# Optimization experiments

Measured on AMD Instinct MI355X. Metric: run time of the kernel, lower is better.

The kernel has to match this reference:

```python
import jax, jax.numpy as jnp
import numpy as np

D_MODEL = 1024
N_EXPERTS = 8
TOP_K = 2
LN_EPS = 1e-5


def setup_inputs() -> dict:
    key = jax.random.key(0)
    ks = jax.random.split(key, 8)
    B, S, d, E = 2, 2048, D_MODEL, N_EXPERTS
    f = 2 * d
    s_in = 0.02
    return {
        "x": jax.random.normal(ks[0], (B, S, d), jnp.float32),
        "Wg": jax.random.normal(ks[1], (d, E), jnp.float32) * s_in,
        "bg": jnp.zeros((E,), jnp.float32),
        "W1": jax.random.normal(ks[2], (E, d, f), jnp.float32) * s_in,
        "b1": jnp.zeros((E, f), jnp.float32),
        "W2": jax.random.normal(ks[3], (E, f, d), jnp.float32) * s_in,
        "b2": jnp.zeros((E, d), jnp.float32),
        "gamma": jnp.ones((d,), jnp.float32),
        "beta": jnp.zeros((d,), jnp.float32),
    }


def reference(x, Wg, bg, W1, b1, W2, b2, gamma, beta):
    # Gating + top-k routing (softmax over the selected top-k logits only)
    logits = jnp.einsum("bsd,de->bse", x, Wg) + bg            # [B,S,E]
    topk_vals, topk_idx = jax.lax.top_k(logits, TOP_K)         # [B,S,K]
    topk_w = jax.nn.softmax(topk_vals, axis=-1)                # [B,S,K]

    # Expert MLPs evaluated densely for all experts (dropout is identity in eval)
    h = jax.nn.relu(jnp.einsum("bsd,edf->bsef", x, W1) + b1)   # [B,S,E,2d]
    eo = jnp.einsum("bsef,efd->bsed", h, W2) + b2              # [B,S,E,d]

    # Gather the top-k experts' outputs per token and combine with gate weights
    sel = jnp.take_along_axis(eo, topk_idx[..., None], axis=2)  # [B,S,K,d]
    mixed = jnp.sum(sel * topk_w[..., None], axis=2)            # [B,S,d]

    # Residual + LayerNorm
    y = mixed + x
    mu = jnp.mean(y, axis=-1, keepdims=True)
    var = jnp.mean(jnp.square(y - mu), axis=-1, keepdims=True)
    return gamma * (y - mu) * jax.lax.rsqrt(var + LN_EPS) + beta
```

## Files before the change

### kernel.cpp

```cpp
#include <hip/hip_runtime.h>


typedef unsigned short ushort_t;
typedef short short8 __attribute__((ext_vector_type(8)));
typedef float f32x4 __attribute__((ext_vector_type(4)));

#define T_TOKENS 4096
#define DMODEL 1024
#define FFN 2048
#define NEXP 8
#define MAXSLOTS 9216
#define GATE_BLOCKS 256
#define TOK_PER_BLK 16

__device__ __forceinline__ ushort_t f2bf(float f) {
    unsigned u = __float_as_uint(f);
    return (ushort_t)((u + 0x7fffu + ((u >> 16) & 1u)) >> 16);
}
__device__ __forceinline__ float bflo(unsigned packed) {
    return __uint_as_float(packed << 16);
}
__device__ __forceinline__ float bfhi(unsigned packed) {
    return __uint_as_float(packed & 0xffff0000u);
}

__device__ __forceinline__ void gload_lds16(const void* g, void* l) {
    __builtin_amdgcn_global_load_lds(
        (const __attribute__((address_space(1))) unsigned int*)g,
        (__attribute__((address_space(3))) unsigned int*)l,
        16, 0, 0);
}

__global__ void init_kernel(int* slot_token) {
    int i = blockIdx.x * 256 + threadIdx.x;
    if (i < MAXSLOTS) slot_token[i] = -1;
}

__global__ __launch_bounds__(256) void gate_kernel(
    const float* __restrict__ x, const float* __restrict__ Wg,
    const float* __restrict__ bg,
    int* __restrict__ top_idx, float* __restrict__ top_w,
    int* __restrict__ blk_hist)
{
    __shared__ int hist[NEXP];
    const int tid = threadIdx.x, lane = tid & 63, w = tid >> 6;
    if (tid < NEXP) hist[tid] = 0;
    __syncthreads();

    float wreg[16][8];
    #pragma unroll
    for (int i = 0; i < 16; i++) {
        const float4* wp = (const float4*)&Wg[(i * 64 + lane) * 8];
        float4 a = wp[0], b = wp[1];
        wreg[i][0] = a.x; wreg[i][1] = a.y; wreg[i][2] = a.z; wreg[i][3] = a.w;
        wreg[i][4] = b.x; wreg[i][5] = b.y; wreg[i][6] = b.z; wreg[i][7] = b.w;
    }
    float bgv[8];
    #pragma unroll
    for (int e = 0; e < 8; e++) bgv[e] = bg[e];

    const int t0 = blockIdx.x * TOK_PER_BLK + w * 4;
    #pragma unroll 1
    for (int it = 0; it < 4; it++) {
        int t = t0 + it;
        const float* xr = x + (size_t)t * DMODEL;
        float acc[8] = {0.f,0.f,0.f,0.f,0.f,0.f,0.f,0.f};
        #pragma unroll
        for (int i = 0; i < 16; i++) {
            float xv = xr[i * 64 + lane];
            #pragma unroll
            for (int e = 0; e < 8; e++) acc[e] += xv * wreg[i][e];
        }
        #pragma unroll
        for (int off = 32; off > 0; off >>= 1) {
            #pragma unroll
            for (int e = 0; e < 8; e++) acc[e] += __shfl_down(acc[e], off);
        }
        if (lane == 0) {
            float l[8];
            #pragma unroll
            for (int e = 0; e < 8; e++) l[e] = acc[e] + bgv[e];
            int i0 = 0; float v0 = l[0];
            #pragma unroll
            for (int e = 1; e < 8; e++) if (l[e] > v0) { v0 = l[e]; i0 = e; }
            int i1 = -1; float v1 = -1e30f;
            #pragma unroll
            for (int e = 0; e < 8; e++) if (e != i0 && l[e] > v1) { v1 = l[e]; i1 = e; }
            float eg = expf(v1 - v0);
            float den = 1.f + eg;
            int p0 = atomicAdd(&hist[i0], 1);
            int p1 = atomicAdd(&hist[i1], 1);
            top_idx[2 * t]     = i0 | (p0 << 4);
            top_idx[2 * t + 1] = i1 | (p1 << 4);
            top_w[2 * t]     = 1.f / den;
            top_w[2 * t + 1] = eg / den;
        }
    }
    __syncthreads();
    if (tid < NEXP) blk_hist[blockIdx.x * NEXP + tid] = hist[tid];
}

__global__ __launch_bounds__(512) void scan_kernel(
    const int* __restrict__ blk_hist, int* __restrict__ blk_base,
    int* __restrict__ offs)
{
    __shared__ int cnt[NEXP];
    const int tid = threadIdx.x, lane = tid & 63, e = tid >> 6;
    int carry = 0;
    #pragma unroll
    for (int r = 0; r < GATE_BLOCKS / 64; r++) {
        int b = r * 64 + lane;
        int orig = blk_hist[b * NEXP + e];
        int v = orig;
        #pragma unroll
        for (int off = 1; off < 64; off <<= 1) {
            int u = __shfl_up(v, off);
            if (lane >= off) v += u;
        }
        blk_base[b * NEXP + e] = carry + v - orig;
        carry += __shfl(v, 63);
    }
    if (lane == 0) cnt[e] = carry;
    __syncthreads();
    if (tid == 0) {
        int cum = 0;
        for (int ee = 0; ee < NEXP; ee++) {
            offs[ee] = cum;
            cum += (cnt[ee] + 127) & ~127;
        }
        offs[NEXP] = cum;
    }
}

__global__ void scatter_kernel(const int* __restrict__ top_idx,
                               const int* __restrict__ offs,
                               const int* __restrict__ blk_base,
                               int* __restrict__ slot_token,
                               int* __restrict__ slot_of)
{
    int t = blockIdx.x * 256 + threadIdx.x;
    if (t >= T_TOKENS) return;
    int gb = t / TOK_PER_BLK;
    #pragma unroll
    for (int k = 0; k < 2; k++) {
        int v = top_idx[2 * t + k];
        int e = v & 15;
        int pos = v >> 4;
        int slot = offs[e] + blk_base[gb * NEXP + e] + pos;
        slot_token[slot] = t;
        slot_of[2 * t + k] = slot;
    }
}

__global__ __launch_bounds__(256) void gather_kernel(
    const float* __restrict__ x, const int* __restrict__ slot_token,
    ushort_t* __restrict__ Xg)
{
    int row = blockIdx.x * 2 + (threadIdx.x >> 7);
    int c = threadIdx.x & 127;
    int tok = slot_token[row];
    uint4* dst = (uint4*)(Xg + (size_t)row * DMODEL) + c;
    if (tok < 0) {
        *dst = make_uint4(0, 0, 0, 0);
        return;
    }
    const float4* sx = (const float4*)(x + (size_t)tok * DMODEL) + c * 2;
    float4 a = sx[0], b = sx[1];
    uint4 o;
    o.x = f2bf(a.x) | ((unsigned)f2bf(a.y) << 16);
    o.y = f2bf(a.z) | ((unsigned)f2bf(a.w) << 16);
    o.z = f2bf(b.x) | ((unsigned)f2bf(b.y) << 16);
    o.w = f2bf(b.z) | ((unsigned)f2bf(b.w) << 16);
    *dst = o;
}

__global__ __launch_bounds__(256) void transpose_kernel(
    const float* __restrict__ src, ushort_t* __restrict__ dst, int R, int C)
{
    __shared__ ushort_t tile[64][68];
    const float* s = src + (size_t)blockIdx.z * R * C;
    ushort_t* d = dst + (size_t)blockIdx.z * R * C;
    int c0 = blockIdx.x * 64, r0 = blockIdx.y * 64;
    int fc = threadIdx.x & 15, rp = threadIdx.x >> 4;
    #pragma unroll
    for (int p = 0; p < 4; p++) {
        int r = p * 16 + rp;
        float4 v = *(const float4*)&s[(size_t)(r0 + r) * C + c0 + fc * 4];
        uint2 pk;
        pk.x = f2bf(v.x) | ((unsigned)f2bf(v.y) << 16);
        pk.y = f2bf(v.z) | ((unsigned)f2bf(v.w) << 16);
        *(uint2*)&tile[r][fc * 4] = pk;
    }
    __syncthreads();
    #pragma unroll
    for (int p = 0; p < 4; p++) {
        int c = p * 16 + rp;
        int rb = fc * 4;
        uint2 pk;
        pk.x = tile[rb + 0][c] | ((unsigned)tile[rb + 1][c] << 16);
        pk.y = tile[rb + 2][c] | ((unsigned)tile[rb + 3][c] << 16);
        *(uint2*)&d[(size_t)(c0 + c) * R + r0 + rb] = pk;
    }
}

template <int K, int N, bool RELU, typename OutT>
__global__ __launch_bounds__(256) void expert_gemm(
    const ushort_t* __restrict__ A,
    const ushort_t* __restrict__ Bt,
    const float* __restrict__ bias,
    OutT* __restrict__ Cout,
    const int* __restrict__ offs)
{
    const int e  = blockIdx.z;
    const int mt = blockIdx.y;
    const int nt = blockIdx.x;
    const int off_e = offs[e];
    const int Mpad  = offs[e + 1] - off_e;
    if (mt * 128 >= Mpad) return;

    __shared__ __align__(16) ushort_t As[128 * 32];
    __shared__ __align__(16) ushort_t Bs[128 * 32];

    const int tid  = threadIdx.x;
    const int lane = tid & 63;
    const int w    = tid >> 6;
    const int quad = lane >> 4;
    const int r16  = lane & 15;
    const int lrow = lane >> 2;
    const int lk   = (lane & 3) * 8;

    const size_t arow0 = (size_t)(off_e + mt * 128);
    const ushort_t* aS0 = A + (arow0 + (size_t)(2 * w + 0) * 16 + lrow) * K + lk;
    const ushort_t* aS1 = A + (arow0 + (size_t)(2 * w + 1) * 16 + lrow) * K + lk;
    const ushort_t* Bte = Bt + (size_t)e * N * K;
    const ushort_t* bS0 = Bte + ((size_t)(nt * 128 + (2 * w + 0) * 16 + lrow)) * K + lk;
    const ushort_t* bS1 = Bte + ((size_t)(nt * 128 + (2 * w + 1) * 16 + lrow)) * K + lk;
    ushort_t* aD0 = &As[(2 * w + 0) * 512];
    ushort_t* aD1 = &As[(2 * w + 1) * 512];
    ushort_t* bD0 = &Bs[(2 * w + 0) * 512];
    ushort_t* bD1 = &Bs[(2 * w + 1) * 512];

    const int wm = (w >> 1) * 64;
    const int wn = (w & 1) * 64;

    f32x4 acc[4][4];
    #pragma unroll
    for (int i = 0; i < 4; i++)
        #pragma unroll
        for (int j = 0; j < 4; j++)
            acc[i][j] = (f32x4){0.f, 0.f, 0.f, 0.f};

    for (int k0 = 0; k0 < K; k0 += 32) {
        gload_lds16(aS0 + k0, aD0);
        gload_lds16(aS1 + k0, aD1);
        gload_lds16(bS0 + k0, bD0);
        gload_lds16(bS1 + k0, bD1);
        __syncthreads();
        short8 af[4], bfr[4];
        #pragma unroll
        for (int i = 0; i < 4; i++)
            af[i] = *(const short8*)&As[(wm + i * 16 + r16) * 32 + quad * 8];
        #pragma unroll
        for (int j = 0; j < 4; j++)
            bfr[j] = *(const short8*)&Bs[(wn + j * 16 + r16) * 32 + quad * 8];
        #pragma unroll
        for (int i = 0; i < 4; i++)
            #pragma unroll
            for (int j = 0; j < 4; j++)
                acc[i][j] = __builtin_amdgcn_mfma_f32_16x16x32_bf16(
                    af[i], bfr[j], acc[i][j], 0, 0, 0);
        __syncthreads();
    }

    const float* be = bias + (size_t)e * N;
    #pragma unroll
    for (int i = 0; i < 4; i++) {
        #pragma unroll
        for (int j = 0; j < 4; j++) {
            int n = nt * 128 + wn + j * 16 + r16;
            float bv = be[n];
            #pragma unroll
            for (int r = 0; r < 4; r++) {
                int m = mt * 128 + wm + i * 16 + quad * 4 + r;
                float v = acc[i][j][r] + bv;
                if (RELU) v = v > 0.f ? v : 0.f;
                size_t idx = (size_t)(off_e + m) * N + n;
                if constexpr (sizeof(OutT) == 2)
                    ((ushort_t*)Cout)[idx] = f2bf(v);
                else
                    ((float*)Cout)[idx] = v;
            }
        }
    }
}

__global__ __launch_bounds__(256) void ln_kernel(
    const float* __restrict__ x, const ushort_t* __restrict__ O,
    const int* __restrict__ slot_of, const float* __restrict__ top_w,
    const float* __restrict__ gamma, const float* __restrict__ beta,
    float* __restrict__ out)
{
    int t = blockIdx.x, tid = threadIdx.x;
    int s0 = slot_of[2 * t], s1 = slot_of[2 * t + 1];
    float w0 = top_w[2 * t], w1 = top_w[2 * t + 1];
    float4 xv = ((const float4*)(x + (size_t)t * DMODEL))[tid];
    uint2 a = ((const uint2*)(O + (size_t)s0 * DMODEL))[tid];
    uint2 b = ((const uint2*)(O + (size_t)s1 * DMODEL))[tid];

    float y[4];
    y[0] = xv.x + w0 * bflo(a.x) + w1 * bflo(b.x);
    y[1] = xv.y + w0 * bfhi(a.x) + w1 * bfhi(b.x);
    y[2] = xv.z + w0 * bflo(a.y) + w1 * bflo(b.y);
    y[3] = xv.w + w0 * bfhi(a.y) + w1 * bfhi(b.y);

    float s = y[0] + y[1] + y[2] + y[3];
    float sq = y[0]*y[0] + y[1]*y[1] + y[2]*y[2] + y[3]*y[3];
    __shared__ float red[2][4];
    #pragma unroll
    for (int off = 32; off > 0; off >>= 1) {
        s += __shfl_down(s, off);
        sq += __shfl_down(sq, off);
    }
    int lane = tid & 63, wv = tid >> 6;
    if (lane == 0) { red[0][wv] = s; red[1][wv] = sq; }
    __syncthreads();
    if (tid == 0) {
        float S = red[0][0] + red[0][1] + red[0][2] + red[0][3];
        float SQ = red[1][0] + red[1][1] + red[1][2] + red[1][3];
        float mu = S * (1.f / DMODEL);
        float var = SQ * (1.f / DMODEL) - mu * mu;
        red[0][0] = mu;
        red[1][0] = rsqrtf(var + 1e-5f);
    }
    __syncthreads();
    float mu = red[0][0], inv = red[1][0];
    float4 gv = ((const float4*)gamma)[tid];
    float4 bv = ((const float4*)beta)[tid];
    float4 ov;
    ov.x = gv.x * (y[0] - mu) * inv + bv.x;
    ov.y = gv.y * (y[1] - mu) * inv + bv.y;
    ov.z = gv.z * (y[2] - mu) * inv + bv.z;
    ov.w = gv.w * (y[3] - mu) * inv + bv.w;
    ((float4*)(out + (size_t)t * DMODEL))[tid] = ov;
}

extern "C" void kernel_launch(void* const* d_in, const int* in_sizes, int n_in,
                              void* d_out, int out_size, void* d_ws, size_t ws_size,
                              hipStream_t stream)
{
    const float* x     = (const float*)d_in[0];
    const float* Wg    = (const float*)d_in[1];
    const float* bg    = (const float*)d_in[2];
    const float* W1    = (const float*)d_in[3];
    const float* b1    = (const float*)d_in[4];
    const float* W2    = (const float*)d_in[5];
    const float* b2    = (const float*)d_in[6];
    const float* gamma = (const float*)d_in[7];
    const float* beta  = (const float*)d_in[8];
    float* out = (float*)d_out;

    char* ws = (char*)d_ws;
    size_t o = 0;
    auto alloc = [&](size_t bytes) {
        size_t r = o;
        o = (o + bytes + 255) & ~(size_t)255;
        return r;
    };
    size_t o_offs    = alloc((NEXP + 1) * 4);
    size_t o_topidx  = alloc((size_t)T_TOKENS * 2 * 4);
    size_t o_topw    = alloc((size_t)T_TOKENS * 2 * 4);
    size_t o_slottok = alloc((size_t)MAXSLOTS * 4);
    size_t o_slotof  = alloc((size_t)T_TOKENS * 2 * 4);
    size_t o_bhist   = alloc((size_t)GATE_BLOCKS * NEXP * 4);
    size_t o_bbase   = alloc((size_t)GATE_BLOCKS * NEXP * 4);
    size_t o_w1t     = alloc((size_t)NEXP * DMODEL * FFN * 2);
    size_t o_w2t     = alloc((size_t)NEXP * DMODEL * FFN * 2);
    size_t o_xg      = alloc((size_t)MAXSLOTS * DMODEL * 2);
    size_t o_h       = alloc((size_t)MAXSLOTS * FFN * 2);
    size_t o_obuf    = alloc((size_t)MAXSLOTS * DMODEL * 2);
    (void)ws_size; (void)in_sizes; (void)n_in; (void)out_size;

    int*      offs       = (int*)(ws + o_offs);
    int*      top_idx    = (int*)(ws + o_topidx);
    float*    top_w      = (float*)(ws + o_topw);
    int*      slot_token = (int*)(ws + o_slottok);
    int*      slot_of    = (int*)(ws + o_slotof);
    int*      blk_hist   = (int*)(ws + o_bhist);
    int*      blk_base   = (int*)(ws + o_bbase);
    ushort_t* W1T        = (ushort_t*)(ws + o_w1t);
    ushort_t* W2T        = (ushort_t*)(ws + o_w2t);
    ushort_t* Xg         = (ushort_t*)(ws + o_xg);
    ushort_t* H          = (ushort_t*)(ws + o_h);
    ushort_t* Obuf       = (ushort_t*)(ws + o_obuf);

    init_kernel<<<MAXSLOTS / 256, 256, 0, stream>>>(slot_token);
    gate_kernel<<<GATE_BLOCKS, 256, 0, stream>>>(x, Wg, bg, top_idx, top_w, blk_hist);
    scan_kernel<<<1, 512, 0, stream>>>(blk_hist, blk_base, offs);
    scatter_kernel<<<T_TOKENS / 256, 256, 0, stream>>>(top_idx, offs, blk_base, slot_token, slot_of);
    gather_kernel<<<MAXSLOTS / 2, 256, 0, stream>>>(x, slot_token, Xg);
    transpose_kernel<<<dim3(FFN / 64, DMODEL / 64, NEXP), 256, 0, stream>>>(W1, W1T, DMODEL, FFN);
    transpose_kernel<<<dim3(DMODEL / 64, FFN / 64, NEXP), 256, 0, stream>>>(W2, W2T, FFN, DMODEL);
    expert_gemm<DMODEL, FFN, true, ushort_t>
        <<<dim3(FFN / 128, 32, NEXP), 256, 0, stream>>>(Xg, W1T, b1, H, offs);
    expert_gemm<FFN, DMODEL, false, ushort_t>
        <<<dim3(DMODEL / 128, 32, NEXP), 256, 0, stream>>>(H, W2T, b2, Obuf, offs);
    ln_kernel<<<T_TOKENS, 256, 0, stream>>>(x, Obuf, slot_of, top_w, gamma, beta, out);
}
```

Baseline: 337.5 us.

## Fuse scatter/gather, merge transposes, swizzle GEMM LDS, reorder grid

```diff
diff --git a/kernel.cpp b/kernel.cpp
--- a/kernel.cpp
+++ b/kernel.cpp
@@ -29,11 +29,6 @@
         (const __attribute__((address_space(1))) unsigned int*)g,
         (__attribute__((address_space(3))) unsigned int*)l,
         16, 0, 0);
-}
-
-__global__ void init_kernel(int* slot_token) {
-    int i = blockIdx.x * 256 + threadIdx.x;
-    if (i < MAXSLOTS) slot_token[i] = -1;
 }
 
 __global__ __launch_bounds__(256) void gate_kernel(
@@ -132,55 +127,52 @@
     }
 }
 
-__global__ void scatter_kernel(const int* __restrict__ top_idx,
-                               const int* __restrict__ offs,
-                               const int* __restrict__ blk_base,
-                               int* __restrict__ slot_token,
-                               int* __restrict__ slot_of)
-{
-    int t = blockIdx.x * 256 + threadIdx.x;
-    if (t >= T_TOKENS) return;
-    int gb = t / TOK_PER_BLK;
-    #pragma unroll
-    for (int k = 0; k < 2; k++) {
-        int v = top_idx[2 * t + k];
-        int e = v & 15;
-        int pos = v >> 4;
+__global__ __launch_bounds__(256) void scatter_gather_kernel(
+    const float* __restrict__ x, const int* __restrict__ top_idx,
+    const int* __restrict__ offs, const int* __restrict__ blk_base,
+    int* __restrict__ slot_of, ushort_t* __restrict__ Xg)
+{
+    const int t = blockIdx.x, tid = threadIdx.x;
+    __shared__ int slots[2];
+    if (tid < 2) {
+        int v = top_idx[2 * t + tid];
+        int e = v & 15, pos = v >> 4;
+        int gb = t / TOK_PER_BLK;
         int slot = offs[e] + blk_base[gb * NEXP + e] + pos;
-        slot_token[slot] = t;
-        slot_of[2 * t + k] = slot;
-    }
-}
-
-__global__ __launch_bounds__(256) void gather_kernel(
-    const float* __restrict__ x, const int* __restrict__ slot_token,
-    ushort_t* __restrict__ Xg)
-{
-    int row = blockIdx.x * 2 + (threadIdx.x >> 7);
-    int c = threadIdx.x & 127;
-    int tok = slot_token[row];
-    uint4* dst = (uint4*)(Xg + (size_t)row * DMODEL) + c;
-    if (tok < 0) {
-        *dst = make_uint4(0, 0, 0, 0);
-        return;
-    }
-    const float4* sx = (const float4*)(x + (size_t)tok * DMODEL) + c * 2;
-    float4 a = sx[0], b = sx[1];
-    uint4 o;
-    o.x = f2bf(a.x) | ((unsigned)f2bf(a.y) << 16);
-    o.y = f2bf(a.z) | ((unsigned)f2bf(a.w) << 16);
-    o.z = f2bf(b.x) | ((unsigned)f2bf(b.y) << 16);
-    o.w = f2bf(b.z) | ((unsigned)f2bf(b.w) << 16);
-    *dst = o;
+        slot_of[2 * t + tid] = slot;
+        slots[tid] = slot;
+    }
+    __syncthreads();
+    float4 xv = ((const float4*)(x + (size_t)t * DMODEL))[tid];
+    uint2 pk;
+    pk.x = f2bf(xv.x) | ((unsigned)f2bf(xv.y) << 16);
+    pk.y = f2bf(xv.z) | ((unsigned)f2bf(xv.w) << 16);
+    ((uint2*)(Xg + (size_t)slots[0] * DMODEL))[tid] = pk;
+    ((uint2*)(Xg + (size_t)slots[1] * DMODEL))[tid] = pk;
 }
 
 __global__ __launch_bounds__(256) void transpose_kernel(
-    const float* __restrict__ src, ushort_t* __restrict__ dst, int R, int C)
+    const float* __restrict__ W1, const float* __restrict__ W2,
+    ushort_t* __restrict__ W1T, ushort_t* __restrict__ W2T)
 {
     __shared__ ushort_t tile[64][68];
-    const float* s = src + (size_t)blockIdx.z * R * C;
-    ushort_t* d = dst + (size_t)blockIdx.z * R * C;
-    int c0 = blockIdx.x * 64, r0 = blockIdx.y * 64;
+    int b = blockIdx.x;
+    const float* s; ushort_t* d; int R, C, rt, ct;
+    if (b < 4096) {
+        int e = b >> 9, t = b & 511;
+        rt = t >> 5; ct = t & 31;
+        s = W1 + (size_t)e * DMODEL * FFN;
+        d = W1T + (size_t)e * DMODEL * FFN;
+        R = DMODEL; C = FFN;
+    } else {
+        b -= 4096;
+        int e = b >> 9, t = b & 511;
+        rt = t >> 4; ct = t & 15;
+        s = W2 + (size_t)e * DMODEL * FFN;
+        d = W2T + (size_t)e * DMODEL * FFN;
+        R = FFN; C = DMODEL;
+    }
+    int r0 = rt * 64, c0 = ct * 64;
     int fc = threadIdx.x & 15, rp = threadIdx.x >> 4;
     #pragma unroll
     for (int p = 0; p < 4; p++) {
@@ -203,17 +195,17 @@
     }
 }
 
-template <int K, int N, bool RELU, typename OutT>
+template <int K, int N, bool RELU>
 __global__ __launch_bounds__(256) void expert_gemm(
     const ushort_t* __restrict__ A,
     const ushort_t* __restrict__ Bt,
     const float* __restrict__ bias,
-    OutT* __restrict__ Cout,
+    ushort_t* __restrict__ Cout,
     const int* __restrict__ offs)
 {
-    const int e  = blockIdx.z;
-    const int mt = blockIdx.y;
-    const int nt = blockIdx.x;
+    const int e  = blockIdx.x;
+    const int nt = blockIdx.y;
+    const int mt = blockIdx.z;
     const int off_e = offs[e];
     const int Mpad  = offs[e + 1] - off_e;
     if (mt * 128 >= Mpad) return;
@@ -227,7 +219,7 @@
     const int quad = lane >> 4;
     const int r16  = lane & 15;
     const int lrow = lane >> 2;
-    const int lk   = (lane & 3) * 8;
+    const int lk   = (((lane & 3) ^ ((lane >> 3) & 3))) * 8;
 
     const size_t arow0 = (size_t)(off_e + mt * 128);
     const ushort_t* aS0 = A + (arow0 + (size_t)(2 * w + 0) * 16 + lrow) * K + lk;
@@ -242,6 +234,7 @@
 
     const int wm = (w >> 1) * 64;
     const int wn = (w & 1) * 64;
+    const int sw = ((r16 >> 1) & 3) ^ quad;
 
     f32x4 acc[4][4];
     #pragma unroll
@@ -259,10 +252,10 @@
         short8 af[4], bfr[4];
         #pragma unroll
         for (int i = 0; i < 4; i++)
-            af[i] = *(const short8*)&As[(wm + i * 16 + r16) * 32 + quad * 8];
+            af[i] = *(const short8*)&As[(wm + i * 16 + r16) * 32 + sw * 8];
         #pragma unroll
         for (int j = 0; j < 4; j++)
-            bfr[j] = *(const short8*)&Bs[(wn + j * 16 + r16) * 32 + quad * 8];
+            bfr[j] = *(const short8*)&Bs[(wn + j * 16 + r16) * 32 + sw * 8];
         #pragma unroll
         for (int i = 0; i < 4; i++)
             #pragma unroll
@@ -284,11 +277,7 @@
                 int m = mt * 128 + wm + i * 16 + quad * 4 + r;
                 float v = acc[i][j][r] + bv;
                 if (RELU) v = v > 0.f ? v : 0.f;
-                size_t idx = (size_t)(off_e + m) * N + n;
-                if constexpr (sizeof(OutT) == 2)
-                    ((ushort_t*)Cout)[idx] = f2bf(v);
-                else
-                    ((float*)Cout)[idx] = v;
+                Cout[(size_t)(off_e + m) * N + n] = f2bf(v);
             }
         }
     }
@@ -369,7 +358,6 @@
     size_t o_offs    = alloc((NEXP + 1) * 4);
     size_t o_topidx  = alloc((size_t)T_TOKENS * 2 * 4);
     size_t o_topw    = alloc((size_t)T_TOKENS * 2 * 4);
-    size_t o_slottok = alloc((size_t)MAXSLOTS * 4);
     size_t o_slotof  = alloc((size_t)T_TOKENS * 2 * 4);
     size_t o_bhist   = alloc((size_t)GATE_BLOCKS * NEXP * 4);
     size_t o_bbase   = alloc((size_t)GATE_BLOCKS * NEXP * 4);
@@ -380,29 +368,25 @@
     size_t o_obuf    = alloc((size_t)MAXSLOTS * DMODEL * 2);
     (void)ws_size; (void)in_sizes; (void)n_in; (void)out_size;
 
-    int*      offs       = (int*)(ws + o_offs);
-    int*      top_idx    = (int*)(ws + o_topidx);
-    float*    top_w      = (float*)(ws + o_topw);
-    int*      slot_token = (int*)(ws + o_slottok);
-    int*      slot_of    = (int*)(ws + o_slotof);
-    int*      blk_hist   = (int*)(ws + o_bhist);
-    int*      blk_base   = (int*)(ws + o_bbase);
-    ushort_t* W1T        = (ushort_t*)(ws + o_w1t);
-    ushort_t* W2T        = (ushort_t*)(ws + o_w2t);
-    ushort_t* Xg         = (ushort_t*)(ws + o_xg);
-    ushort_t* H          = (ushort_t*)(ws + o_h);
-    ushort_t* Obuf       = (ushort_t*)(ws + o_obuf);
-
-    init_kernel<<<MAXSLOTS / 256, 256, 0, stream>>>(slot_token);
+    int*      offs     = (int*)(ws + o_offs);
+    int*      top_idx  = (int*)(ws + o_topidx);
+    float*    top_w    = (float*)(ws + o_topw);
+    int*      slot_of  = (int*)(ws + o_slotof);
+    int*      blk_hist = (int*)(ws + o_bhist);
+    int*      blk_base = (int*)(ws + o_bbase);
+    ushort_t* W1T      = (ushort_t*)(ws + o_w1t);
+    ushort_t* W2T      = (ushort_t*)(ws + o_w2t);
+    ushort_t* Xg       = (ushort_t*)(ws + o_xg);
+    ushort_t* H        = (ushort_t*)(ws + o_h);
+    ushort_t* Obuf     = (ushort_t*)(ws + o_obuf);
+
     gate_kernel<<<GATE_BLOCKS, 256, 0, stream>>>(x, Wg, bg, top_idx, top_w, blk_hist);
+    transpose_kernel<<<8192, 256, 0, stream>>>(W1, W2, W1T, W2T);
     scan_kernel<<<1, 512, 0, stream>>>(blk_hist, blk_base, offs);
-    scatter_kernel<<<T_TOKENS / 256, 256, 0, stream>>>(top_idx, offs, blk_base, slot_token, slot_of);
-    gather_kernel<<<MAXSLOTS / 2, 256, 0, stream>>>(x, slot_token, Xg);
-    transpose_kernel<<<dim3(FFN / 64, DMODEL / 64, NEXP), 256, 0, stream>>>(W1, W1T, DMODEL, FFN);
-    transpose_kernel<<<dim3(DMODEL / 64, FFN / 64, NEXP), 256, 0, stream>>>(W2, W2T, FFN, DMODEL);
-    expert_gemm<DMODEL, FFN, true, ushort_t>
-        <<<dim3(FFN / 128, 32, NEXP), 256, 0, stream>>>(Xg, W1T, b1, H, offs);
-    expert_gemm<FFN, DMODEL, false, ushort_t>
-        <<<dim3(DMODEL / 128, 32, NEXP), 256, 0, stream>>>(H, W2T, b2, Obuf, offs);
+    scatter_gather_kernel<<<T_TOKENS, 256, 0, stream>>>(x, top_idx, offs, blk_base, slot_of, Xg);
+    expert_gemm<DMODEL, FFN, true>
+        <<<dim3(NEXP, FFN / 128, 32), 256, 0, stream>>>(Xg, W1T, b1, H, offs);
+    expert_gemm<FFN, DMODEL, false>
+        <<<dim3(NEXP, DMODEL / 128, 32), 256, 0, stream>>>(H, W2T, b2, Obuf, offs);
     ln_kernel<<<T_TOKENS, 256, 0, stream>>>(x, Obuf, slot_of, top_w, gamma, beta, out);
 }
```

After: 316.3 us. -6.3%, faster.
